# Optimization experiments

Hardware: AMD Instinct MI355X
Metric: run time of the kernel (lower is better)

Reference implementation:

```python
import jax, jax.numpy as jnp
import numpy as np

IN_CAPS = 1152
OUT_CAPS = 10
IN_DIM = 8
OUT_DIM = 16
ROUTING_ITERS = 3
BATCH = 512


def squash(s, axis=-1, eps=1e-8):
    # v = (||s||^2 / (1 + ||s||^2)) * s / ||s||
    mag_sq = jnp.sum(s * s, axis=axis, keepdims=True)
    mag = jnp.sqrt(mag_sq + eps)
    return (mag_sq / (1.0 + mag_sq)) * (s / mag)


def setup_inputs() -> dict:
    key = jax.random.key(0)
    kx, kw = jax.random.split(key)
    x = jax.random.normal(kx, (BATCH, IN_CAPS, IN_DIM), dtype=jnp.float32)
    stdv = 1.0 / np.sqrt(IN_CAPS)
    W = jax.random.uniform(kw, (IN_CAPS, OUT_CAPS, OUT_DIM, IN_DIM),
                           minval=-stdv, maxval=stdv, dtype=jnp.float32)
    return {"x": x, "W": W}


def reference(x, W):
    # u_hat[b,i,j,:] = W[i,j] @ x[b,i]  -> [B, 1152, 10, 16]
    u_hat = jnp.einsum('ijde,bie->bijd', W, x)
    u_det = jax.lax.stop_gradient(u_hat)
    b = jnp.zeros((x.shape[0], IN_CAPS, OUT_CAPS), dtype=x.dtype)
    v = None
    for it in range(ROUTING_ITERS):
        c = jax.nn.softmax(b, axis=2)  # softmax over out capsules
        u = u_hat if it == ROUTING_ITERS - 1 else u_det
        s = jnp.einsum('bij,bijd->bjd', c, u)  # [B, 10, 16]
        v = squash(s, axis=-1)
        if it != ROUTING_ITERS - 1:
            # agreement: u_hat . v  -> [B, 1152, 10]
            b = b + jnp.einsum('bijd,bjd->bij', u_det, v)
    return v  # [B, 10, 16]
```

## Files before the change

kernel.cpp:

```cpp
#include <hip/hip_runtime.h>
#include <math.h>

#define J 10
#define BT 16
#define NBT 32
#define NIC 16
#define ICB 72
#define IPW 18
#define JD 160
#define BATCH 512
#define IN_CAPS 1152
#define RTH 256

typedef __attribute__((ext_vector_type(8))) short short8;
typedef __attribute__((ext_vector_type(4))) float f32x4;

__device__ inline short f2bf(float f) {
    union { float f; unsigned u; } v; v.f = f;
    return (short)((v.u + 0x7FFFu + ((v.u >> 16) & 1u)) >> 16);
}
__device__ inline short8 cvt8(float4 a, float4 b) {
    short8 o;
    o[0] = f2bf(a.x); o[1] = f2bf(a.y); o[2] = f2bf(a.z); o[3] = f2bf(a.w);
    o[4] = f2bf(b.x); o[5] = f2bf(b.y); o[6] = f2bf(b.z); o[7] = f2bf(b.w);
    return o;
}

__global__ __launch_bounds__(256) void convert_w(
    const float* __restrict__ W, short* __restrict__ Wb, short* __restrict__ zb)
{
    const int t = blockIdx.x * 256 + threadIdx.x;
    const float4* src = (const float4*)W + (size_t)t * 2;
    *(short8*)(Wb + (size_t)t * 8) = cvt8(src[0], src[1]);
    if (blockIdx.x == 0 && threadIdx.x < 32) zb[threadIdx.x] = 0;
}

#define TI 32
#define TB 64
__global__ __launch_bounds__(256) void transpose_x(
    const float* __restrict__ X, short* __restrict__ Xb)
{
    __shared__ short8 tile[TI][TB + 1];
    const int it = blockIdx.x % (IN_CAPS / TI);
    const int bt = blockIdx.x / (IN_CAPS / TI);
    const int t  = threadIdx.x;

    const int i_l = t & 31, b_s = t >> 5;
#pragma unroll
    for (int p = 0; p < 8; ++p) {
        const int b_l = p * 8 + b_s;
        const float4* src = (const float4*)(X +
            (((size_t)(bt * TB + b_l)) * IN_CAPS + it * TI + i_l) * 8);
        tile[i_l][b_l] = cvt8(src[0], src[1]);
    }
    __syncthreads();
    const int b_l = t & 63, i_s = t >> 6;
#pragma unroll
    for (int p = 0; p < 8; ++p) {
        const int i_l2 = p * 4 + i_s;
        *(short8*)(Xb + (((size_t)(it * TI + i_l2)) * BATCH + bt * TB + b_l) * 8)
            = tile[i_l2][b_l];
    }
}

template<int MODE>
__global__ __launch_bounds__(RTH, 2) void route_kernel(
    const short* __restrict__ Xb, const short* __restrict__ Wb,
    const short* __restrict__ zb, const float* __restrict__ V,
    float* __restrict__ S_part)
{
    __shared__ float s_lds[BT][JD + 1];
    const int tid   = threadIdx.x;
    const int lane  = tid & 63, wave = tid >> 6;
    const int icb   = blockIdx.x % NIC;
    const int btile = blockIdx.x / NIC;
    const int bcol  = lane & 15, kg = lane >> 4;
    const int b     = btile * BT + bcol;

    for (int t = tid; t < BT * (JD + 1); t += RTH) (&s_lds[0][0])[t] = 0.f;
    __syncthreads();

    if (MODE == 0) {
        f32x4 acc[J];
#pragma unroll
        for (int j = 0; j < J; ++j) acc[j] = (f32x4)(0.f);
        for (int ks = wave; ks < ICB / 4; ks += 4) {
            const int ia = icb * ICB + ks * 4 + kg;
            const short8 bfr = *(const short8*)(Xb + ((size_t)ia * BATCH + b) * 8);
            short8 afr[J];
#pragma unroll
            for (int j = 0; j < J; ++j)
                afr[j] = *(const short8*)(Wb + (size_t)ia * 1280 + j * 128 + bcol * 8);
#pragma unroll
            for (int j = 0; j < J; ++j)
                acc[j] = __builtin_amdgcn_mfma_f32_16x16x32_bf16(afr[j], bfr, acc[j], 0, 0, 0);
        }
#pragma unroll
        for (int j = 0; j < J; ++j)
#pragma unroll
            for (int r = 0; r < 4; ++r)
                atomicAdd(&s_lds[bcol][j * 16 + kg * 4 + r], 0.1f * acc[j][r]);
    } else {
        float4 Vr[J];
#pragma unroll
        for (int j = 0; j < J; ++j)
            Vr[j] = *(const float4*)(V + (size_t)b * JD + j * 16 + kg * 4);

        float s_acc[J][4];
#pragma unroll
        for (int j = 0; j < J; ++j)
#pragma unroll
            for (int r = 0; r < 4; ++r) s_acc[j][r] = 0.f;

        const int i0w = icb * ICB + wave * IPW;
        const short8 zero8 = (short8)(short)0;

#pragma unroll
        for (int g = 0; g < 5; ++g) {
            const int nt = (g < 4) ? 4 : 2;
            int ia = i0w + g * 4 + kg;
            if (ia > IN_CAPS - 1) ia = IN_CAPS - 1;

            short8 afr[J];
#pragma unroll
            for (int j = 0; j < J; ++j)
                afr[j] = *(const short8*)(Wb + (size_t)ia * 1280 + j * 128 + bcol * 8);
            const short8 bfull = *(const short8*)(Xb + ((size_t)ia * BATCH + b) * 8);

            for (int t = 0; t < nt; ++t) {
                const short8 bt = (kg == t) ? bfull : zero8;
                f32x4 u[J];
#pragma unroll
                for (int j = 0; j < J; ++j)
                    u[j] = __builtin_amdgcn_mfma_f32_16x16x32_bf16(afr[j], bt, (f32x4)(0.f), 0, 0, 0);

                float L[J];
#pragma unroll
                for (int j = 0; j < J; ++j)
                    L[j] = u[j][0] * Vr[j].x + u[j][1] * Vr[j].y
                         + u[j][2] * Vr[j].z + u[j][3] * Vr[j].w;
#pragma unroll
                for (int j = 0; j < J; ++j) {
                    L[j] += __shfl_xor(L[j], 16);
                    L[j] += __shfl_xor(L[j], 32);
                }
                float c[J], Z = 0.f;
#pragma unroll
                for (int j = 0; j < J; ++j) { c[j] = __expf(L[j]); Z += c[j]; }
                const float rz = 1.0f / Z;
#pragma unroll
                for (int j = 0; j < J; ++j) {
                    const float cj = c[j] * rz;
                    s_acc[j][0] += cj * u[j][0];
                    s_acc[j][1] += cj * u[j][1];
                    s_acc[j][2] += cj * u[j][2];
                    s_acc[j][3] += cj * u[j][3];
                }
            }
        }
#pragma unroll
        for (int j = 0; j < J; ++j)
#pragma unroll
            for (int r = 0; r < 4; ++r)
                atomicAdd(&s_lds[bcol][j * 16 + kg * 4 + r], s_acc[j][r]);
    }
    __syncthreads();

    for (int t = tid; t < BT * JD; t += RTH) {
        const int bb = t / JD, p = t % JD;
        S_part[((size_t)icb * BATCH + btile * BT + bb) * JD + p] = s_lds[bb][p];
    }
}

__global__ __launch_bounds__(256) void squash_kernel(
    const float* __restrict__ S_part, float* __restrict__ V,
    float* __restrict__ out, int mode)
{
    const int t = blockIdx.x * 256 + threadIdx.x;
    float s = 0.f;
#pragma unroll
    for (int ic = 0; ic < NIC; ic++)
        s += S_part[(size_t)ic * BATCH * JD + t];
    float sq = s * s;
    sq += __shfl_xor(sq, 1);
    sq += __shfl_xor(sq, 2);
    sq += __shfl_xor(sq, 4);
    sq += __shfl_xor(sq, 8);
    const float v = s * sq / ((1.f + sq) * sqrtf(sq + 1e-8f));
    if (mode == 0)      V[t] = v;
    else if (mode == 1) V[t] += v;
    else                out[t] = v;
}

extern "C" void kernel_launch(void* const* d_in, const int* in_sizes, int n_in,
                              void* d_out, int out_size, void* d_ws, size_t ws_size,
                              hipStream_t stream)
{
    const float* X = (const float*)d_in[0];
    const float* W = (const float*)d_in[1];
    float* out = (float*)d_out;

    float* S_part = (float*)d_ws;
    float* V      = S_part + (size_t)NIC * BATCH * JD;
    short* Wb     = (short*)(V + (size_t)BATCH * JD);
    short* Xb     = Wb + (size_t)IN_CAPS * JD * 8;
    short* zb     = Xb + (size_t)IN_CAPS * BATCH * 8;

    const dim3 rg(NBT * NIC), rb(RTH);
    const dim3 sg(BATCH * JD / 256), sb(256);

    convert_w<<<dim3(720), dim3(256), 0, stream>>>(W, Wb, zb);
    transpose_x<<<dim3((IN_CAPS / TI) * (BATCH / TB)), dim3(256), 0, stream>>>(X, Xb);

    route_kernel<0><<<rg, rb, 0, stream>>>(Xb, Wb, zb, V, S_part);
    squash_kernel<<<sg, sb, 0, stream>>>(S_part, V, out, 0);
    route_kernel<1><<<rg, rb, 0, stream>>>(Xb, Wb, zb, V, S_part);
    squash_kernel<<<sg, sb, 0, stream>>>(S_part, V, out, 1);
    route_kernel<1><<<rg, rb, 0, stream>>>(Xb, Wb, zb, V, S_part);
    squash_kernel<<<sg, sb, 0, stream>>>(S_part, V, out, 2);
}
```

Baseline: 151.7 us.

## Fold routing coefficients into scaled x and accumulate s via MFMA

In the routing passes, the weighted sum over input capsules is no longer done by per-element FMAs on u_hat. Each lane now scales its x vector by its own softmax coefficient, packs it to bf16, and issues one accumulating MFMA per output capsule. This uses the linearity of W·x to cut the VALU work per group of four input capsules. In exchange it rounds c·x to bf16, which adds precision error, and it computes all four softmaxes per group before selecting the one that belongs to each lane.

Measured after the change: 156.6 us. 1.03x slower.

```diff
diff --git a/kernel.cpp b/kernel.cpp
--- a/kernel.cpp
+++ b/kernel.cpp
@@ -14,6 +14,7 @@
 
 typedef __attribute__((ext_vector_type(8))) short short8;
 typedef __attribute__((ext_vector_type(4))) float f32x4;
+typedef __attribute__((ext_vector_type(4))) unsigned uint4v;
 
 __device__ inline short f2bf(float f) {
     union { float f; unsigned u; } v; v.f = f;
@@ -24,6 +25,10 @@
     o[0] = f2bf(a.x); o[1] = f2bf(a.y); o[2] = f2bf(a.z); o[3] = f2bf(a.w);
     o[4] = f2bf(b.x); o[5] = f2bf(b.y); o[6] = f2bf(b.z); o[7] = f2bf(b.w);
     return o;
+}
+__device__ inline float bf2f(short s) {
+    union { unsigned u; float f; } v; v.u = ((unsigned)(unsigned short)s) << 16;
+    return v.f;
 }
 
 __global__ __launch_bounds__(256) void convert_w(
@@ -106,11 +111,9 @@
         for (int j = 0; j < J; ++j)
             Vr[j] = *(const float4*)(V + (size_t)b * JD + j * 16 + kg * 4);
 
-        float s_acc[J][4];
-#pragma unroll
-        for (int j = 0; j < J; ++j)
-#pragma unroll
-            for (int r = 0; r < 4; ++r) s_acc[j][r] = 0.f;
+        f32x4 acc[J];
+#pragma unroll
+        for (int j = 0; j < J; ++j) acc[j] = (f32x4)(0.f);
 
         const int i0w = icb * ICB + wave * IPW;
         const short8 zero8 = (short8)(short)0;
@@ -127,42 +130,72 @@
                 afr[j] = *(const short8*)(Wb + (size_t)ia * 1280 + j * 128 + bcol * 8);
             const short8 bfull = *(const short8*)(Xb + ((size_t)ia * BATCH + b) * 8);
 
-            for (int t = 0; t < nt; ++t) {
-                const short8 bt = (kg == t) ? bfull : zero8;
-                f32x4 u[J];
-#pragma unroll
-                for (int j = 0; j < J; ++j)
-                    u[j] = __builtin_amdgcn_mfma_f32_16x16x32_bf16(afr[j], bt, (f32x4)(0.f), 0, 0, 0);
-
-                float L[J];
-#pragma unroll
-                for (int j = 0; j < J; ++j)
-                    L[j] = u[j][0] * Vr[j].x + u[j][1] * Vr[j].y
-                         + u[j][2] * Vr[j].z + u[j][3] * Vr[j].w;
-#pragma unroll
-                for (int j = 0; j < J; ++j) {
-                    L[j] += __shfl_xor(L[j], 16);
-                    L[j] += __shfl_xor(L[j], 32);
-                }
-                float c[J], Z = 0.f;
-#pragma unroll
-                for (int j = 0; j < J; ++j) { c[j] = __expf(L[j]); Z += c[j]; }
-                const float rz = 1.0f / Z;
-#pragma unroll
-                for (int j = 0; j < J; ++j) {
-                    const float cj = c[j] * rz;
-                    s_acc[j][0] += cj * u[j][0];
-                    s_acc[j][1] += cj * u[j][1];
-                    s_acc[j][2] += cj * u[j][2];
-                    s_acc[j][3] += cj * u[j][3];
+            float xf[8];
+#pragma unroll
+            for (int e = 0; e < 8; ++e) xf[e] = bf2f(bfull[e]);
+
+            float Lp[4][J];
+#pragma unroll
+            for (int t = 0; t < 4; ++t) {
+                if (t < nt) {
+                    const short8 bt = (kg == t) ? bfull : zero8;
+#pragma unroll
+                    for (int j = 0; j < J; ++j) {
+                        const f32x4 u = __builtin_amdgcn_mfma_f32_16x16x32_bf16(
+                            afr[j], bt, (f32x4)(0.f), 0, 0, 0);
+                        Lp[t][j] = u[0] * Vr[j].x + u[1] * Vr[j].y
+                                 + u[2] * Vr[j].z + u[3] * Vr[j].w;
+                    }
                 }
             }
+
+            float cSel[J];
+#pragma unroll
+            for (int j = 0; j < J; ++j) cSel[j] = 0.f;
+#pragma unroll
+            for (int t = 0; t < 4; ++t) {
+                if (t < nt) {
+                    float c[J], Z = 0.f;
+#pragma unroll
+                    for (int j = 0; j < J; ++j) {
+                        float l = Lp[t][j];
+                        l += __shfl_xor(l, 16);
+                        l += __shfl_xor(l, 32);
+                        c[j] = __expf(l);
+                        Z += c[j];
+                    }
+                    const float rz = 1.0f / Z;
+#pragma unroll
+                    for (int j = 0; j < J; ++j) {
+                        const float cv = c[j] * rz;
+                        cSel[j] = (kg == t) ? cv : cSel[j];
+                    }
+                }
+            }
+
+#pragma unroll
+            for (int j = 0; j < J; ++j) {
+                const float cj = cSel[j];
+                unsigned q0, q1, q2, q3;
+                asm("v_cvt_pk_bf16_f32 %0, %1, %2" : "=v"(q0)
+                    : "v"(xf[0] * cj), "v"(xf[1] * cj));
+                asm("v_cvt_pk_bf16_f32 %0, %1, %2" : "=v"(q1)
+                    : "v"(xf[2] * cj), "v"(xf[3] * cj));
+                asm("v_cvt_pk_bf16_f32 %0, %1, %2" : "=v"(q2)
+                    : "v"(xf[4] * cj), "v"(xf[5] * cj));
+                asm("v_cvt_pk_bf16_f32 %0, %1, %2" : "=v"(q3)
+                    : "v"(xf[6] * cj), "v"(xf[7] * cj));
+                union { uint4v v; short8 s; } bu;
+                bu.v = (uint4v){q0, q1, q2, q3};
+                acc[j] = __builtin_amdgcn_mfma_f32_16x16x32_bf16(
+                    afr[j], bu.s, acc[j], 0, 0, 0);
+            }
         }
 #pragma unroll
         for (int j = 0; j < J; ++j)
 #pragma unroll
             for (int r = 0; r < 4; ++r)
-                atomicAdd(&s_lds[bcol][j * 16 + kg * 4 + r], s_acc[j][r]);
+                atomicAdd(&s_lds[bcol][j * 16 + kg * 4 + r], acc[j][r]);
     }
     __syncthreads();
 
```
